# Performance work log

Hardware: AMD Instinct MI355X
Metric: run time of the kernel (lower is better)

Reference implementation:

```python
import jax, jax.numpy as jnp
import numpy as np

B, N, C, H = 8, 512, 64, 128
T, K = 10, 2                       # dilation threshold and skip divisor
TAUS = (0.25, 0.5, 0.75)
WTS = (0.25, 0.5, 0.25)
EPS_GIN = 0.0                      # (1 + eps) * x, eps buffer
AVG_DEG = 32.0


def setup_inputs() -> dict:
    key = jax.random.key(0)
    ks = jax.random.split(key, 6)
    x = jax.random.normal(ks[0], (B, N, C), jnp.float32)
    u = jax.random.uniform(ks[1], (B, N, N))
    a = u < (AVG_DEG / N)
    adj = jnp.maximum(a, jnp.swapaxes(a, 1, 2)).astype(jnp.float32)  # symmetric binary adjacency
    mask = jax.random.bernoulli(ks[2], 0.9, (B, N))
    W1 = jax.random.normal(ks[3], (C, H), jnp.float32) / np.float32(np.sqrt(C))
    b1 = jnp.zeros((H,), jnp.float32)
    W2 = jax.random.normal(ks[4], (H, C), jnp.float32) / np.float32(np.sqrt(H))
    b2 = jnp.zeros((C,), jnp.float32)
    return {"x": x, "adj": adj, "mask": mask, "W1": W1, "b1": b1, "W2": W2, "b2": b2}


def reference(x, adj, mask, W1, b1, W2, b2):
    Bc, Nc, Cc = x.shape
    eye = jnp.eye(Nc, dtype=bool)
    adj_ = jnp.where(eye, 1.0, adj)                 # add_loop=True: force self loops
    # ---- vectorized dilation (replaces the per-(b,n) python loop) ----
    neigh = (adj_ > 0) & (~eye)                     # neighbors excluding self [B,N,N]
    ni = neigh.astype(jnp.int32)
    rank = jnp.cumsum(ni, axis=-1) - ni             # exclusive rank of m among n's sorted neighbors
    nb = ni.sum(-1)                                 # [B,N] neighbor count (w/o self)
    skip = jnp.where(nb > T, (nb + K - 1) // K, 1)  # ceil(nb/k) if nb > T else 1 (linear mode, layer 1)
    skip = jnp.maximum(skip, 1)
    sk = skip[:, :, None]
    # remove relative indices skip-1, 2*skip-1, ... when skip > 1, only for masked-in nodes
    rem = neigh & (sk > 1) & ((rank % sk) == (sk - 1)) & mask[:, :, None]
    rem = rem | jnp.swapaxes(rem, 1, 2)             # symmetric removal
    adj_d = jnp.where(rem, 0.0, adj_)
    # ---- masked quantile aggregation over neighbors (== nanquantile) ----
    nd = adj_d > 0                                  # includes self loop -> at least 1 valid
    vals = jnp.where(nd[..., None], x[:, None, :, :], jnp.inf)  # [B,N,M,C]; invalid -> +inf
    s = jnp.sort(vals, axis=2)                      # valid values first, ascending
    nv = nd.sum(2)                                  # [B,N] valid count per node
    agg = jnp.zeros_like(x)
    for tau, w in zip(TAUS, WTS):                   # small fixed loop over quantiles
        pos = jnp.asarray(tau, x.dtype) * jnp.maximum(nv - 1, 0).astype(x.dtype)
        lo = jnp.floor(pos).astype(jnp.int32)
        hi = jnp.ceil(pos).astype(jnp.int32)
        frac = (pos - lo.astype(x.dtype))[..., None]
        idx_lo = jnp.broadcast_to(lo[:, :, None, None], (Bc, Nc, 1, Cc))
        idx_hi = jnp.broadcast_to(hi[:, :, None, None], (Bc, Nc, 1, Cc))
        v_lo = jnp.take_along_axis(s, idx_lo, axis=2)[:, :, 0, :]
        v_hi = jnp.take_along_axis(s, idx_hi, axis=2)[:, :, 0, :]
        agg = agg + jnp.asarray(w, x.dtype) * (v_lo + frac * (v_hi - v_lo))
    agg = jnp.where(nv[..., None] > 0, agg, 0.0)    # nan_to_num for empty rows
    out = (1.0 + EPS_GIN) * x + agg
    h = jax.nn.relu(out @ W1 + b1)                  # GIN MLP: Linear-ReLU-Linear
    y = h @ W2 + b2
    return y * mask[..., None].astype(y.dtype)
```

## Files before the change

### kernel.cpp

```cpp
#include <hip/hip_runtime.h>
#include <cstdint>

#define B_ 8
#define N_ 512
#define C_ 64
#define H_ 128
#define T_ 10
#define K_ 2
#define WPR 16
#define NVMAX 96
#define TT 8

__device__ inline uint32_t fkey(float v) {
    uint32_t bits = __float_as_uint(v);
    return (bits & 0x80000000u) ? ~bits : (bits | 0x80000000u);
}
__device__ inline float fdec(uint32_t key) {
    uint32_t ok = (key & 0xFFFFFF00u) | 0x80u;
    uint32_t bits = (ok & 0x80000000u) ? (ok ^ 0x80000000u) : ~ok;
    return __uint_as_float(bits);
}

__global__ __launch_bounds__(256) void pass1_rem(const float* __restrict__ adj,
                                                 const int* __restrict__ mask,
                                                 uint32_t* __restrict__ rembits) {
    int wid = threadIdx.x >> 6, lane = threadIdx.x & 63;
    int row = blockIdx.x * 4 + wid;
    int i = row & (N_ - 1);
    const float4* arow4 = (const float4*)(adj + (size_t)row * N_);
    float4 a0 = arow4[lane * 2];
    float4 a1 = arow4[lane * 2 + 1];
    float av[8] = {a0.x, a0.y, a0.z, a0.w, a1.x, a1.y, a1.z, a1.w};

    int flags = 0, cnt = 0;
    int jbase = lane * 8;
#pragma unroll
    for (int k = 0; k < 8; ++k) {
        int j = jbase + k;
        bool ng = (j != i) && (av[k] > 0.0f);
        flags |= ((int)ng) << k;
        cnt += (int)ng;
    }
    int inc = cnt;
#pragma unroll
    for (int d = 1; d < 64; d <<= 1) {
        int o = __shfl_up(inc, d, 64);
        if (lane >= d) inc += o;
    }
    int excl = inc - cnt;
    int nb = __shfl(inc, 63, 64);
    int skip = (nb > T_) ? ((nb + K_ - 1) / K_) : 1;
    if (skip < 1) skip = 1;
    int maski = mask[row];

    unsigned byteval = 0;
    if (skip > 1 && maski != 0) {
        int r = excl;
#pragma unroll
        for (int k = 0; k < 8; ++k) {
            if ((flags >> k) & 1) {
                if (r % skip == skip - 1) byteval |= 1u << k;
                ++r;
            }
        }
    }
    unsigned b0 = __shfl((int)byteval, (lane & 15) * 4 + 0, 64);
    unsigned b1 = __shfl((int)byteval, (lane & 15) * 4 + 1, 64);
    unsigned b2 = __shfl((int)byteval, (lane & 15) * 4 + 2, 64);
    unsigned b3 = __shfl((int)byteval, (lane & 15) * 4 + 3, 64);
    if (lane < WPR) {
        uint32_t w = b0 | (b1 << 8) | (b2 << 16) | (b3 << 24);
        rembits[(size_t)row * WPR + lane] = w;
    }
}

__global__ __launch_bounds__(256) void pass2_quant_mlp(
        const float* __restrict__ x, const float* __restrict__ adj,
        const int* __restrict__ mask, const uint32_t* __restrict__ rembits,
        const float* __restrict__ W1, const float* __restrict__ b1,
        const float* __restrict__ W2, const float* __restrict__ b2,
        float* __restrict__ out) {
    int row = blockIdx.x;
    int b = row >> 9, i = row & (N_ - 1);
    int tid = threadIdx.x;
    int lane = tid & 63;
    int q = tid >> 6;

    __shared__ unsigned short kept[NVMAX];
    __shared__ int s_cnt;
    __shared__ uint32_t keys[NVMAX * C_];
    __shared__ float selv[6][C_];
    __shared__ int s_rr[6];
    __shared__ float s_frac[3];
    __shared__ float out_node[C_];
    __shared__ float hbuf[H_];

    if (tid == 0) s_cnt = 0;
    __syncthreads();

    const float* arow = adj + (size_t)row * N_;
    const uint32_t* rrow = rembits + (size_t)row * WPR;
    const uint32_t* rbase = rembits + (size_t)(b * N_) * WPR;

    for (int jb = 0; jb < N_; jb += 256) {
        int j = jb + tid;
        bool keep;
        if (j == i) {
            keep = true;
        } else {
            keep = (arow[j] > 0.0f);
            if (keep) {
                unsigned rij = (rrow[j >> 5] >> (j & 31)) & 1u;
                unsigned rji = (rbase[(size_t)j * WPR + (i >> 5)] >> (i & 31)) & 1u;
                keep = ((rij | rji) == 0u);
            }
        }
        unsigned long long bal = __ballot(keep);
        int base = 0;
        if (lane == 0 && bal) base = atomicAdd(&s_cnt, __popcll(bal));
        base = __shfl(base, 0, 64);
        if (keep) {
            int pos = __popcll(bal & ((1ull << lane) - 1ull));
            int p = base + pos;
            if (p < NVMAX) kept[p] = (unsigned short)j;
        }
    }
    __syncthreads();
    int nv = s_cnt;
    if (nv > NVMAX) nv = NVMAX;

    const float* xb = x + (size_t)b * N_ * C_;

    for (int t = q; t < nv; t += 4) {
        float v = xb[(size_t)kept[t] * C_ + lane];
        keys[t * C_ + lane] = (fkey(v) & 0xFFFFFF00u) | (uint32_t)t;
    }

    if (tid == 0) {
        const float taus[3] = {0.25f, 0.5f, 0.75f};
        float nm1 = (float)((nv - 1 > 0) ? nv - 1 : 0);
        for (int qq = 0; qq < 3; ++qq) {
            float pos = taus[qq] * nm1;
            int lo = (int)floorf(pos);
            int hi = (int)ceilf(pos);
            s_rr[2 * qq] = lo; s_rr[2 * qq + 1] = hi;
            s_frac[qq] = pos - (float)lo;
        }
    }
    __syncthreads();

    int rr0 = s_rr[0], rr1 = s_rr[1], rr2 = s_rr[2],
        rr3 = s_rr[3], rr4 = s_rr[4], rr5 = s_rr[5];

    const uint32_t* kcol = keys + lane;

    for (int base = 0; base < nv; base += 32) {
        int tbase = base + q * TT;
        if (tbase >= nv) continue;
        uint32_t k[TT];
        int rs_a[TT], rs_b[TT];
#pragma unroll
        for (int m = 0; m < TT; ++m) {
            int t = tbase + m;
            k[m] = (t < nv) ? kcol[t * C_] : 0xFFFFFFFFu;
            rs_a[m] = 0; rs_b[m] = 0;
        }
        int u = 0;
#pragma unroll 2
        for (; u + 1 < nv; u += 2) {
            uint32_t w0 = kcol[u * C_];
            uint32_t w1 = kcol[(u + 1) * C_];
#pragma unroll
            for (int m = 0; m < TT; ++m) {
                rs_a[m] += (int)(w0 < k[m]);
                rs_b[m] += (int)(w1 < k[m]);
            }
        }
        if (u < nv) {
            uint32_t w0 = kcol[u * C_];
#pragma unroll
            for (int m = 0; m < TT; ++m) rs_a[m] += (int)(w0 < k[m]);
        }
#pragma unroll
        for (int m = 0; m < TT; ++m) {
            int rs = rs_a[m] + rs_b[m];
            bool h0 = rs == rr0, h1 = rs == rr1, h2 = rs == rr2;
            bool h3 = rs == rr3, h4 = rs == rr4, h5 = rs == rr5;
            if (h0 | h1 | h2 | h3 | h4 | h5) {
                float fv = fdec(k[m]);
                if (h0) selv[0][lane] = fv;
                if (h1) selv[1][lane] = fv;
                if (h2) selv[2][lane] = fv;
                if (h3) selv[3][lane] = fv;
                if (h4) selv[4][lane] = fv;
                if (h5) selv[5][lane] = fv;
            }
        }
    }
    __syncthreads();

    if (tid < C_) {
        float f0 = s_frac[0], f1 = s_frac[1], f2 = s_frac[2];
        float agg = 0.25f * (selv[0][tid] + f0 * (selv[1][tid] - selv[0][tid]));
        agg      += 0.5f  * (selv[2][tid] + f1 * (selv[3][tid] - selv[2][tid]));
        agg      += 0.25f * (selv[4][tid] + f2 * (selv[5][tid] - selv[4][tid]));
        out_node[tid] = xb[(size_t)i * C_ + tid] + agg;
    }
    __syncthreads();

    float maskf = (mask[row] != 0) ? 1.0f : 0.0f;
    if (tid < H_) {
        float acc = b1[tid];
        for (int c = 0; c < C_; ++c) acc += out_node[c] * W1[c * H_ + tid];
        hbuf[tid] = acc > 0.0f ? acc : 0.0f;
    }
    __syncthreads();
    if (tid < C_) {
        float acc = b2[tid];
        for (int k = 0; k < H_; ++k) acc += hbuf[k] * W2[k * C_ + tid];
        out[(size_t)row * C_ + tid] = acc * maskf;
    }
}

extern "C" void kernel_launch(void* const* d_in, const int* in_sizes, int n_in,
                              void* d_out, int out_size, void* d_ws, size_t ws_size,
                              hipStream_t stream) {
    const float* x   = (const float*)d_in[0];
    const float* adj = (const float*)d_in[1];
    const int*  mask = (const int*)d_in[2];
    const float* W1  = (const float*)d_in[3];
    const float* b1  = (const float*)d_in[4];
    const float* W2  = (const float*)d_in[5];
    const float* b2  = (const float*)d_in[6];
    float* out = (float*)d_out;

    uint32_t* rembits = (uint32_t*)d_ws;

    hipLaunchKernelGGL(pass1_rem, dim3(B_ * N_ / 4), dim3(256), 0, stream,
                       adj, mask, rembits);
    hipLaunchKernelGGL(pass2_quant_mlp, dim3(B_ * N_), dim3(256), 0, stream,
                       x, adj, mask, rembits, W1, b1, W2, b2, out);
}
```

Measured before the change: 165.6 us.

## Split rank-select into two 32-channel passes to halve key smem footprint

The quantile rank-counting stage now processes the 64 channels in two groups of 32. Each wavefront splits into two half-waves working on different candidate slots, so the shared key buffer shrinks from 96x64 to 96x32 words. This cuts LDS use per block to allow more resident blocks, but costs an extra gather-and-sync phase. Pass1 also drops the per-element modulo in favour of a running counter that resets at each removal.

```diff
diff --git a/kernel.cpp b/kernel.cpp
--- a/kernel.cpp
+++ b/kernel.cpp
@@ -10,6 +10,7 @@
 #define WPR 16
 #define NVMAX 96
 #define TT 8
+#define CG 32
 
 __device__ inline uint32_t fkey(float v) {
     uint32_t bits = __float_as_uint(v);
@@ -55,12 +56,12 @@
 
     unsigned byteval = 0;
     if (skip > 1 && maski != 0) {
-        int r = excl;
+        int r = excl % skip;
 #pragma unroll
         for (int k = 0; k < 8; ++k) {
             if ((flags >> k) & 1) {
-                if (r % skip == skip - 1) byteval |= 1u << k;
-                ++r;
+                if (r == skip - 1) { byteval |= 1u << k; r = 0; }
+                else ++r;
             }
         }
     }
@@ -85,10 +86,12 @@
     int tid = threadIdx.x;
     int lane = tid & 63;
     int q = tid >> 6;
+    int c = lane & 31;
+    int g = lane >> 5;
 
     __shared__ unsigned short kept[NVMAX];
     __shared__ int s_cnt;
-    __shared__ uint32_t keys[NVMAX * C_];
+    __shared__ uint32_t keys[NVMAX * CG];
     __shared__ float selv[6][C_];
     __shared__ int s_rr[6];
     __shared__ float s_frac[3];
@@ -131,11 +134,6 @@
 
     const float* xb = x + (size_t)b * N_ * C_;
 
-    for (int t = q; t < nv; t += 4) {
-        float v = xb[(size_t)kept[t] * C_ + lane];
-        keys[t * C_ + lane] = (fkey(v) & 0xFFFFFF00u) | (uint32_t)t;
-    }
-
     if (tid == 0) {
         const float taus[3] = {0.25f, 0.5f, 0.75f};
         float nm1 = (float)((nv - 1 > 0) ? nv - 1 : 0);
@@ -152,52 +150,62 @@
     int rr0 = s_rr[0], rr1 = s_rr[1], rr2 = s_rr[2],
         rr3 = s_rr[3], rr4 = s_rr[4], rr5 = s_rr[5];
 
-    const uint32_t* kcol = keys + lane;
-
-    for (int base = 0; base < nv; base += 32) {
-        int tbase = base + q * TT;
-        if (tbase >= nv) continue;
-        uint32_t k[TT];
-        int rs_a[TT], rs_b[TT];
-#pragma unroll
-        for (int m = 0; m < TT; ++m) {
-            int t = tbase + m;
-            k[m] = (t < nv) ? kcol[t * C_] : 0xFFFFFFFFu;
-            rs_a[m] = 0; rs_b[m] = 0;
-        }
-        int u = 0;
+    const uint32_t* kcol = keys + c;
+
+    for (int grp = 0; grp < 2; ++grp) {
+        for (int f = tid; f < nv * CG; f += 256) {
+            int t = f >> 5, cc = f & 31;
+            float v = xb[(size_t)kept[t] * C_ + grp * CG + cc];
+            keys[t * CG + cc] = (fkey(v) & 0xFFFFFF00u) | (uint32_t)t;
+        }
+        __syncthreads();
+
+        for (int base = 0; base < nv; base += 64) {
+            int wslot = base + q * 16;
+            if (wslot >= nv) continue;
+            int tbase = wslot + g * TT;
+            uint32_t k[TT];
+            int rs_a[TT], rs_b[TT];
+#pragma unroll
+            for (int m = 0; m < TT; ++m) {
+                int t = tbase + m;
+                k[m] = (t < nv) ? kcol[t * CG] : 0xFFFFFFFFu;
+                rs_a[m] = 0; rs_b[m] = 0;
+            }
+            int u = 0;
 #pragma unroll 2
-        for (; u + 1 < nv; u += 2) {
-            uint32_t w0 = kcol[u * C_];
-            uint32_t w1 = kcol[(u + 1) * C_];
+            for (; u + 1 < nv; u += 2) {
+                uint32_t w0 = kcol[u * CG];
+                uint32_t w1 = kcol[(u + 1) * CG];
+#pragma unroll
+                for (int m = 0; m < TT; ++m) {
+                    rs_a[m] += (int)(w0 < k[m]);
+                    rs_b[m] += (int)(w1 < k[m]);
+                }
+            }
+            if (u < nv) {
+                uint32_t w0 = kcol[u * CG];
+#pragma unroll
+                for (int m = 0; m < TT; ++m) rs_a[m] += (int)(w0 < k[m]);
+            }
 #pragma unroll
             for (int m = 0; m < TT; ++m) {
-                rs_a[m] += (int)(w0 < k[m]);
-                rs_b[m] += (int)(w1 < k[m]);
-            }
-        }
-        if (u < nv) {
-            uint32_t w0 = kcol[u * C_];
-#pragma unroll
-            for (int m = 0; m < TT; ++m) rs_a[m] += (int)(w0 < k[m]);
-        }
-#pragma unroll
-        for (int m = 0; m < TT; ++m) {
-            int rs = rs_a[m] + rs_b[m];
-            bool h0 = rs == rr0, h1 = rs == rr1, h2 = rs == rr2;
-            bool h3 = rs == rr3, h4 = rs == rr4, h5 = rs == rr5;
-            if (h0 | h1 | h2 | h3 | h4 | h5) {
-                float fv = fdec(k[m]);
-                if (h0) selv[0][lane] = fv;
-                if (h1) selv[1][lane] = fv;
-                if (h2) selv[2][lane] = fv;
-                if (h3) selv[3][lane] = fv;
-                if (h4) selv[4][lane] = fv;
-                if (h5) selv[5][lane] = fv;
-            }
-        }
-    }
-    __syncthreads();
+                int rs = rs_a[m] + rs_b[m];
+                bool h0 = rs == rr0, h1 = rs == rr1, h2 = rs == rr2;
+                bool h3 = rs == rr3, h4 = rs == rr4, h5 = rs == rr5;
+                if (h0 | h1 | h2 | h3 | h4 | h5) {
+                    float fv = fdec(k[m]);
+                    if (h0) selv[0][grp * CG + c] = fv;
+                    if (h1) selv[1][grp * CG + c] = fv;
+                    if (h2) selv[2][grp * CG + c] = fv;
+                    if (h3) selv[3][grp * CG + c] = fv;
+                    if (h4) selv[4][grp * CG + c] = fv;
+                    if (h5) selv[5][grp * CG + c] = fv;
+                }
+            }
+        }
+        __syncthreads();
+    }
 
     if (tid < C_) {
         float f0 = s_frac[0], f1 = s_frac[1], f2 = s_frac[2];
@@ -211,7 +219,7 @@
     float maskf = (mask[row] != 0) ? 1.0f : 0.0f;
     if (tid < H_) {
         float acc = b1[tid];
-        for (int c = 0; c < C_; ++c) acc += out_node[c] * W1[c * H_ + tid];
+        for (int cc = 0; cc < C_; ++cc) acc += out_node[cc] * W1[cc * H_ + tid];
         hbuf[tid] = acc > 0.0f ? acc : 0.0f;
     }
     __syncthreads();
```

After: 173.0 us. 4.5% more time.
